# Kernel optimization log

Hardware: AMD Instinct MI355X
Metric: run time of the kernel (lower is better)

Reference implementation:

```python
import jax, jax.numpy as jnp
import numpy as np

CHUNK = 2048  # output-direction chunk size for the fused score+reduce scan


def _stereographic_normals(out_size):
    # matches torch.meshgrid default (ij indexing): v = rows, u = cols
    v, u = jnp.meshgrid(jnp.arange(out_size, dtype=jnp.float32),
                        jnp.arange(out_size, dtype=jnp.float32), indexing='ij')
    p = 4.0 * ((u + 0.5) / out_size - 0.5)
    q = -4.0 * ((v + 0.5) / out_size - 0.5)
    d = 1.0 + p ** 2 + q ** 2
    x = 2.0 * p / d
    y = 2.0 * q / d
    z = -(-1.0 + p ** 2 + q ** 2) / d
    return jnp.stack([x, y, z], axis=-1).reshape(-1, 3)  # [out_size^2, 3]


def _forward(image, normal_map, mask, kappa, out_size):
    B, C, H, W = image.shape
    N = H * W
    k = jnp.float32(kappa)
    coef = k / (2.0 * jnp.pi * (1.0 - jnp.exp(-2.0 * k)))  # vMF normalization

    V = image.reshape(B, C, N).transpose(0, 2, 1)              # [B,N,C]
    n_in = normal_map.reshape(B, 3, N).transpose(0, 2, 1)      # [B,N,3]
    w = (mask.reshape(B, N) > 0).astype(image.dtype)[..., None]  # 0/1 validity
    # fuse numerator (v^2) and denominator (v) accumulations into one pass
    Vaug = jnp.concatenate([V * w, (V ** 2) * w], axis=-1)     # [B,N,2C]

    M = _stereographic_normals(out_size)                        # [N_out,3]
    n_chunks = M.shape[0] // CHUNK
    chunks = M.reshape(n_chunks, CHUNK, 3)

    def body(carry, Mc):
        dp = jnp.einsum('bnd,cd->bnc', n_in, Mc)                # cos similarity
        f = coef * jnp.exp(-k * (1.0 - dp))                     # vMF kernel
        return carry, jnp.einsum('bnc,bnk->bck', f, Vaug)       # [B,CHUNK,2C]

    _, outs = jax.lax.scan(jax.checkpoint(body), 0.0, chunks)   # [n_chunks,B,CHUNK,2C]
    vals = outs.transpose(1, 0, 2, 3).reshape(B, out_size * out_size, 2 * C)
    s, num = vals[..., :C], vals[..., C:]
    out_pixels = num / (s + 0.001)                              # [B,N_out,C]
    return out_pixels.transpose(0, 2, 1).reshape(B, C, out_size, out_size)


def setup_inputs() -> dict:
    key = jax.random.key(0)
    k1, k2, k3 = jax.random.split(key, 3)
    B, C, H, W = 2, 3, 128, 128
    image = jax.random.uniform(k1, (B, C, H, W), dtype=jnp.float32)
    nm = jax.random.normal(k2, (B, 3, H, W), dtype=jnp.float32)
    nm = nm / jnp.linalg.norm(nm, axis=1, keepdims=True)  # unit normals
    mask = jax.random.randint(k3, (B, H, W), 0, 2).astype(jnp.int32)
    return {"image": image, "normal_map": nm, "mask": mask,
            "kappa": 100, "out_size": 256}


def reference(image, normal_map, mask, kappa, out_size):
    return _forward(image, normal_map, mask, kappa, out_size)
```

## Files before the change

kernel.cpp:

```cpp
#include <hip/hip_runtime.h>
#include <math.h>

#define B_     2
#define C_     3
#define N_     16384
#define OS_    256
#define OUT_   65536
#define NZ_    32
#define NF_    64
#define NB_    2048
#define NITEM_ 1536
#define GRIDM_ 2048
#define CAP_   16384
#define SP2_   512
#define VSTR_  520
#define TAU_   8.0f
#define LOG2E  1.44269504088896340736f
#define PI_    3.14159265358979323846f

typedef float    f32x4 __attribute__((ext_vector_type(4)));
typedef float    v2f   __attribute__((ext_vector_type(2)));
typedef _Float16 f16x8 __attribute__((ext_vector_type(8)));
typedef __fp16   h16x2 __attribute__((ext_vector_type(2)));

static __device__ __forceinline__ v2f pk_fma(v2f a, v2f b, v2f c) {
    return __builtin_elementwise_fma(a, b, c);
}

__device__ __forceinline__ int pixel_bin(float nx, float ny, float nz) {
    int zi = (int)((nz + 1.0f) * (NZ_ * 0.5f));
    zi = min(max(zi, 0), NZ_ - 1);
    float phi = atan2f(ny, nx);
    int fi = (int)((phi + PI_) * (NF_ / (2.0f * PI_)));
    fi = min(max(fi, 0), NF_ - 1);
    return zi * NF_ + fi;
}

__global__ __launch_bounds__(1024) void hist_scan_kernel(
    const float* __restrict__ nm, const int* __restrict__ mask,
    int* __restrict__ binStart, int* __restrict__ off)
{
    __shared__ int hist[NB_];
    int b = blockIdx.x;
    int tid = threadIdx.x;

    for (int i = tid; i < NB_; i += 1024) hist[i] = 0;
    __syncthreads();

#pragma unroll
    for (int j = 0; j < N_ / 1024; j++) {
        int n = j * 1024 + tid;
        if (mask[b * N_ + n] > 0) {
            const float* nb = nm + (size_t)b * 3 * N_ + n;
            atomicAdd(&hist[pixel_bin(nb[0], nb[N_], nb[2 * N_])], 1);
        }
    }
    __syncthreads();

    if (tid >= 64) return;
    int lane = tid;
    const int per = NB_ / 64;
    int base = lane * per;

    int sum = 0;
#pragma unroll
    for (int i = 0; i < per; i++) sum += hist[base + i];

    int inc = sum;
#pragma unroll
    for (int o = 1; o < 64; o <<= 1) {
        int t = __shfl_up(inc, o);
        if (lane >= o) inc += t;
    }
    int acc = inc - sum;

#pragma unroll
    for (int i = 0; i < per; i++) {
        binStart[b * (NB_ + 1) + base + i] = acc;
        off[b * NB_ + base + i] = acc;
        acc += hist[base + i];
    }
    if (lane == 63) binStart[b * (NB_ + 1) + NB_] = acc;
}

__global__ __launch_bounds__(256) void scatter_plan_kernel(
    const float* __restrict__ img, const float* __restrict__ nm,
    const int* __restrict__ mask, const int* __restrict__ kappa,
    const int* __restrict__ binStart, int* __restrict__ off,
    float* __restrict__ gn, _Float16* __restrict__ gv,
    int* __restrict__ plan, int* __restrict__ tileLen)
{
    int tid = threadIdx.x;
    int bid = blockIdx.x;
    float k = (float)kappa[0];
    float k2 = k * LOG2E;

    if (bid < 128) {
        int idx = bid * 256 + tid;
        if (idx >= B_ * N_) return;
        if (mask[idx] <= 0) return;
        int b = idx / N_, n = idx - b * N_;
        const float* nb = nm + (size_t)b * 3 * N_ + n;
        float nx = nb[0], ny = nb[N_], nz = nb[2 * N_];
        int bin = pixel_bin(nx, ny, nz);
        int pos = atomicAdd(&off[b * NB_ + bin], 1);
        const float* ib = img + (size_t)b * C_ * N_ + n;
        float v0 = ib[0], v1 = ib[N_], v2 = ib[2 * N_];
        gn[((size_t)b * 3 + 0) * CAP_ + pos] = k2 * nx;
        gn[((size_t)b * 3 + 1) * CAP_ + pos] = k2 * ny;
        gn[((size_t)b * 3 + 2) * CAP_ + pos] = k2 * nz;
        _Float16* gvb = gv + (size_t)b * 6 * CAP_;
        gvb[0 * CAP_ + pos] = (_Float16)v0;
        gvb[1 * CAP_ + pos] = (_Float16)v1;
        gvb[2 * CAP_ + pos] = (_Float16)v2;
        gvb[3 * CAP_ + pos] = (_Float16)(v0 * v0);
        gvb[4 * CAP_ + pos] = (_Float16)(v1 * v1);
        gvb[5 * CAP_ + pos] = (_Float16)(v2 * v2);
        return;
    }

    __shared__ int warr[4];
    int bt = bid - 128;
    int b = bt >> 8, tile = bt & 255;
    int tu = tile & 15, tv = tile >> 4;
    int w = tid >> 6, lane = tid & 63;

    float pc  = 4.0f * ((tu * 16 + 8.0f) * (1.0f / OS_) - 0.5f);
    float qc  = -4.0f * ((tv * 16 + 8.0f) * (1.0f / OS_) - 0.5f);
    float ppc = pc * pc + qc * qc, invc = 1.0f / (1.0f + ppc);
    float Tx = 2.0f * pc * invc, Ty = 2.0f * qc * invc, Tz = (1.0f - ppc) * invc;

    float ctile = 1.0f;
#pragma unroll
    for (int j = 0; j < 4; j++) {
        int cl = j * 64 + lane;
        int u = tu * 16 + (cl & 15), v = tv * 16 + (cl >> 4);
        float p = 4.0f * ((u + 0.5f) * (1.0f / OS_) - 0.5f);
        float q = -4.0f * ((v + 0.5f) * (1.0f / OS_) - 0.5f);
        float pp = p * p + q * q;
        float inv = 1.0f / (1.0f + pp);
        float mx = 2.0f * p * inv, my = 2.0f * q * inv, mz = (1.0f - pp) * inv;
        ctile = fminf(ctile, mx * Tx + my * Ty + mz * Tz);
    }
#pragma unroll
    for (int o = 32; o; o >>= 1) ctile = fminf(ctile, __shfl_xor(ctile, o));

    float dpthr = fminf(fmaxf(1.0f - TAU_ / k, -1.0f), 1.0f);
    ctile = fminf(fmaxf(ctile, -1.0f), 1.0f);
    float theta = acosf(dpthr) + acosf(ctile);
    float rhs = (theta >= PI_) ? -2.0f : cosf(theta);

    float rT   = sqrtf(Tx * Tx + Ty * Ty);
    float phiT = atan2f(Ty, Tx);
    int fiT = min(max((int)((phiT + PI_) * (NF_ / (2.0f * PI_))), 0), NF_ - 1);

    const int* bs = binStart + b * (NB_ + 1);
    int Lacc = 0;

#pragma unroll
    for (int j = 0; j < 8; j++) {
        int zi = w + j * 4;
        float z0 = -1.0f + zi * (2.0f / NZ_);
        float z1 = z0 + (2.0f / NZ_);
        float hw  = PI_ / NF_;
        float mid = -PI_ + (2.0f * PI_ / NF_) * lane + hw;
        float d = phiT - mid;
        d = d - (2.0f * PI_) * rintf(d * (0.5f / PI_));
        d = fabsf(d);
        float cmax = (d <= hw) ? 1.0f : cosf(d - hw);
        float A  = rT * cmax;
        float g0 = A * sqrtf(fmaxf(0.0f, 1.0f - z0 * z0)) + Tz * z0;
        float g1 = A * sqrtf(fmaxf(0.0f, 1.0f - z1 * z1)) + Tz * z1;
        float gm = fmaxf(g0, g1);
        if (A > 0.0f) {
            float s2 = A * A + Tz * Tz;
            float zs = Tz * rsqrtf(s2);
            if (zs > z0 && zs < z1) gm = sqrtf(s2);
        }
        unsigned long long m = __ballot(gm >= rhs);

        int base = zi * NF_;
        int st0 = 0, en0 = 0, st1 = 0, en1 = 0;
        if (m) {
            bool full = (~m == 0ull) || !((m >> fiT) & 1ull);
            if (!full) {
                unsigned long long r = fiT ? ((m >> fiT) | (m << (64 - fiT))) : m;
                unsigned long long nr = ~r;
                int bcnt = __builtin_ctzll(nr);
                int acnt = __builtin_clzll(nr);
                if (bcnt + acnt >= NF_) full = true;
                else {
                    int lo = fiT - acnt, hi = fiT + bcnt - 1;
                    if (lo >= 0 && hi < NF_) {
                        st0 = bs[base + lo]; en0 = bs[base + hi + 1];
                    } else if (lo < 0) {
                        st0 = bs[base];            en0 = bs[base + hi + 1];
                        st1 = bs[base + lo + NF_]; en1 = bs[base + NF_];
                    } else {
                        st0 = bs[base];       en0 = bs[base + hi - NF_ + 1];
                        st1 = bs[base + lo];  en1 = bs[base + NF_];
                    }
                }
            }
            if (full) { st0 = bs[base]; en0 = bs[base + NF_]; }
        }
        Lacc += (en0 - st0) + (en1 - st1);
        if (lane == 0) {
            int* o = plan + ((size_t)bt * NZ_ + zi) * 4;
            o[0] = st0; o[1] = en0; o[2] = st1; o[3] = en1;
        }
    }
    if (lane == 0) warr[w] = Lacc;
    __syncthreads();
    if (tid == 0) tileLen[bt] = warr[0] + warr[1] + warr[2] + warr[3];
}

__global__ __launch_bounds__(256) void builder_kernel(
    const int* __restrict__ tileLen, int* __restrict__ tileItemStart,
    int* __restrict__ items, int* __restrict__ hdr)
{
    __shared__ int lds[256];
    int t = threadIdx.x;
    int bt0 = t * 2, bt1 = t * 2 + 1;
    int L0 = tileLen[bt0], L1 = tileLen[bt1];

    lds[t] = L0 + L1;
    __syncthreads();
    for (int o = 128; o > 0; o >>= 1) {
        if (t < o) lds[t] += lds[t + o];
        __syncthreads();
    }
    int SL = lds[0];
    __syncthreads();

    int R = (SL + NITEM_ - 1) / NITEM_;
    if (R < 32) R = 32;

    int P0 = (L0 + R - 1) / R, P1 = (L1 + R - 1) / R;
    int ps = P0 + P1;
    lds[t] = ps;
    __syncthreads();
    for (int o = 1; o < 256; o <<= 1) {
        int v = (t >= o) ? lds[t - o] : 0;
        __syncthreads();
        lds[t] += v;
        __syncthreads();
    }
    int excl  = lds[t] - ps;
    int total = lds[255];

    tileItemStart[bt0] = excl;
    tileItemStart[bt1] = excl + P0;
    if (t == 255) tileItemStart[512] = total;
    if (t == 0)   hdr[0] = R;

    for (int p = 0; p < P0; p++) items[excl + p]      = (bt0 << 12) | p;
    for (int p = 0; p < P1; p++) items[excl + P0 + p] = (bt1 << 12) | p;
    for (int i = total + t; i < GRIDM_; i += 256) items[i] = -1;
}

__global__ __launch_bounds__(256) void main_kernel(
    const float* __restrict__ gn, const _Float16* __restrict__ gv,
    const int* __restrict__ plan, const int* __restrict__ items,
    const int* __restrict__ hdr, const int* __restrict__ kappa,
    float* __restrict__ part2)
{
    __shared__ float    s_nx[SP2_], s_ny[SP2_], s_nz[SP2_];
    __shared__ _Float16 s_va[6 * VSTR_ + 8];
    __shared__ int      rTab[128];
    __shared__ int      sTot;

    int item = items[blockIdx.x];
    if (item < 0) return;
    int bt = item >> 12, piece = item & 4095;
    int tile = bt & 255, b = bt >> 8;
    int tu = tile & 15, tv = tile >> 4;
    int tid = threadIdx.x, w = tid >> 6, lane = tid & 63;

    if (tid < 64) {
        int st = plan[(size_t)bt * (NZ_ * 4) + 2 * tid];
        int en = plan[(size_t)bt * (NZ_ * 4) + 2 * tid + 1];
        int len = en - st; if (len < 0) len = 0;
        int inc = len;
#pragma unroll
        for (int o = 1; o < 64; o <<= 1) {
            int t2 = __shfl_up(inc, o);
            if (tid >= o) inc += t2;
        }
        int pos = inc - len;
        rTab[tid * 2]     = pos;
        rTab[tid * 2 + 1] = st - pos;
        if (tid == 63) sTot = inc;
    }
    if (tid >= 64 && tid < 72) s_va[6 * VSTR_ + (tid - 64)] = (_Float16)0.0f;
    __syncthreads();

    int R   = hdr[0];
    int tot = sTot;
    int plo = piece * R;
    int phi = min(tot, plo + R);

    float k2 = (float)kappa[0] * LOG2E;
    v2f mk2v = {-k2, -k2};

    v2f Mx2[4], My2[4], Mz2[4];
#pragma unroll
    for (int t = 0; t < 4; t++) {
        int u = tu * 16 + (lane & 15);
        int v = tv * 16 + w * 4 + t;
        float p  = 4.0f * ((u + 0.5f) * (1.0f / OS_) - 0.5f);
        float q  = -4.0f * ((v + 0.5f) * (1.0f / OS_) - 0.5f);
        float pp = p * p + q * q;
        float inv = 1.0f / (1.0f + pp);
        float mx = 2.0f * p * inv, my = 2.0f * q * inv, mz = (1.0f - pp) * inv;
        Mx2[t] = (v2f){mx, mx}; My2[t] = (v2f){my, my}; Mz2[t] = (v2f){mz, mz};
    }

    f32x4 acc[4];
#pragma unroll
    for (int t = 0; t < 4; t++) acc[t] = (f32x4){0.0f, 0.0f, 0.0f, 0.0f};

    const float* gnx = gn + ((size_t)b * 3 + 0) * CAP_;
    const float* gny = gn + ((size_t)b * 3 + 1) * CAP_;
    const float* gnz = gn + ((size_t)b * 3 + 2) * CAP_;
    const _Float16* gvb = gv + (size_t)b * 6 * CAP_;

    int ch   = lane & 15;
    int kgrp = (lane >> 4) * 8;

    for (int s0 = plo; s0 < phi; s0 += SP2_) {
        int sp  = min(SP2_, phi - s0);
        int spP = (sp + 31) & ~31;
        int g0i = -1, g1i = -1;
        {
            int f0 = tid;
            if (f0 < sp) {
                int cp = s0 + f0, r = 0;
#pragma unroll
                for (int step = 32; step; step >>= 1) {
                    int nr = r + step;
                    if (rTab[nr * 2] <= cp) r = nr;
                }
                g0i = cp + rTab[r * 2 + 1];
            }
            int f1 = tid + 256;
            if (f1 < sp) {
                int cp = s0 + f1, r = 0;
#pragma unroll
                for (int step = 32; step; step >>= 1) {
                    int nr = r + step;
                    if (rTab[nr * 2] <= cp) r = nr;
                }
                g1i = cp + rTab[r * 2 + 1];
            }
        }
        __syncthreads();
#pragma unroll
        for (int h = 0; h < 2; h++) {
            int f = tid + h * 256;
            int g = h ? g1i : g0i;
            if (f >= spP) break;
            if (g >= 0) {
                s_nx[f] = gnx[g]; s_ny[f] = gny[g]; s_nz[f] = gnz[g];
#pragma unroll
                for (int c2 = 0; c2 < 6; c2++) s_va[c2 * VSTR_ + f] = gvb[c2 * CAP_ + g];
            } else {
                s_nx[f] = 0.0f; s_ny[f] = 0.0f; s_nz[f] = 0.0f;
#pragma unroll
                for (int c2 = 0; c2 < 6; c2++) s_va[c2 * VSTR_ + f] = (_Float16)0.0f;
            }
        }
        __syncthreads();

        for (int k0 = 0; k0 < spP; k0 += 32) {
            int kr = k0 + kgrp;
            const v2f* xv = (const v2f*)&s_nx[kr];
            const v2f* yv = (const v2f*)&s_ny[kr];
            const v2f* zv = (const v2f*)&s_nz[kr];
            v2f x01 = xv[0], x23 = xv[1], x45 = xv[2], x67 = xv[3];
            v2f y01 = yv[0], y23 = yv[1], y45 = yv[2], y67 = yv[3];
            v2f z01 = zv[0], z23 = zv[1], z45 = zv[2], z67 = zv[3];
            f16x8 bfrag;
            if (ch < 6) bfrag = *(const f16x8*)&s_va[ch * VSTR_ + kr];
            else        bfrag = *(const f16x8*)&s_va[6 * VSTR_];
#pragma unroll
            for (int t = 0; t < 4; t++) {
                v2f g01 = pk_fma(x01, Mx2[t], pk_fma(y01, My2[t], pk_fma(z01, Mz2[t], mk2v)));
                v2f g23 = pk_fma(x23, Mx2[t], pk_fma(y23, My2[t], pk_fma(z23, Mz2[t], mk2v)));
                v2f g45 = pk_fma(x45, Mx2[t], pk_fma(y45, My2[t], pk_fma(z45, Mz2[t], mk2v)));
                v2f g67 = pk_fma(x67, Mx2[t], pk_fma(y67, My2[t], pk_fma(z67, Mz2[t], mk2v)));
                h16x2 p0 = __builtin_amdgcn_cvt_pkrtz(__builtin_amdgcn_exp2f(g01.x),
                                                      __builtin_amdgcn_exp2f(g01.y));
                h16x2 p1 = __builtin_amdgcn_cvt_pkrtz(__builtin_amdgcn_exp2f(g23.x),
                                                      __builtin_amdgcn_exp2f(g23.y));
                h16x2 p2 = __builtin_amdgcn_cvt_pkrtz(__builtin_amdgcn_exp2f(g45.x),
                                                      __builtin_amdgcn_exp2f(g45.y));
                h16x2 p3 = __builtin_amdgcn_cvt_pkrtz(__builtin_amdgcn_exp2f(g67.x),
                                                      __builtin_amdgcn_exp2f(g67.y));
                f16x8 afrag;
                afrag[0] = (_Float16)p0[0]; afrag[1] = (_Float16)p0[1];
                afrag[2] = (_Float16)p1[0]; afrag[3] = (_Float16)p1[1];
                afrag[4] = (_Float16)p2[0]; afrag[5] = (_Float16)p2[1];
                afrag[6] = (_Float16)p3[0]; afrag[7] = (_Float16)p3[1];
                acc[t] = __builtin_amdgcn_mfma_f32_16x16x32_f16(afrag, bfrag, acc[t], 0, 0, 0);
            }
        }
        __syncthreads();
    }

    if (ch < 6) {
        float* dst = part2 + (size_t)blockIdx.x * 1536;
#pragma unroll
        for (int t = 0; t < 4; t++) {
#pragma unroll
            for (int r = 0; r < 4; r++) {
                int d = w * 64 + t * 16 + ((lane >> 4) * 4 + r);
                dst[d * 6 + ch] = acc[t][r];
            }
        }
    }
}

__global__ __launch_bounds__(256) void finalize_kernel(
    const float* __restrict__ part2, const int* __restrict__ tileItemStart,
    const int* __restrict__ kappa, float* __restrict__ out)
{
    int idx = blockIdx.x * 256 + threadIdx.x;
    if (idx >= B_ * OUT_) return;
    int b = idx / OUT_;
    int c = idx - b * OUT_;
    int u = c & 255, v = c >> 8;
    int bt = b * 256 + ((v >> 4) * 16 + (u >> 4));
    int cl = (v & 15) * 16 + (u & 15);

    float k = (float)kappa[0];
    float coef = k / (2.0f * PI_ * (1.0f - expf(-2.0f * k)));

    int is0 = tileItemStart[bt], is1 = tileItemStart[bt + 1];
    float s[6] = {0, 0, 0, 0, 0, 0};
    for (int it = is0; it < is1; it++) {
        const float* p = part2 + (size_t)it * 1536 + cl * 6;
#pragma unroll
        for (int i = 0; i < 6; i++) s[i] += p[i];
    }
#pragma unroll
    for (int ch = 0; ch < C_; ch++) {
        out[((size_t)(b * C_ + ch)) * OUT_ + c] = (coef * s[3 + ch]) / (coef * s[ch] + 0.001f);
    }
}

extern "C" void kernel_launch(void* const* d_in, const int* in_sizes, int n_in,
                              void* d_out, int out_size, void* d_ws, size_t ws_size,
                              hipStream_t stream)
{
    const float* img   = (const float*)d_in[0];
    const float* nm    = (const float*)d_in[1];
    const int*   mask  = (const int*)d_in[2];
    const int*   kappa = (const int*)d_in[3];
    float* out = (float*)d_out;

    char* ws = (char*)d_ws;
    size_t o = 0;
    float*     gn        = (float*)(ws + o);     o += (size_t)B_ * 3 * CAP_ * 4;
    _Float16*  gv        = (_Float16*)(ws + o); o += (size_t)B_ * 6 * CAP_ * 2;
    float*     part2     = (float*)(ws + o);     o += (size_t)GRIDM_ * 1536 * 4;
    int* plan            = (int*)(ws + o);       o += (size_t)512 * NZ_ * 4 * 4;
    int* off             = (int*)(ws + o);       o += (size_t)B_ * NB_ * 4;
    int* binStart        = (int*)(ws + o);       o += ((size_t)B_ * (NB_ + 1) * 4 + 15) & ~15ull;
    int* tileLen         = (int*)(ws + o);       o += 512 * 4;
    int* tileItemStart   = (int*)(ws + o);       o += (513 * 4 + 15) & ~15ull;
    int* items           = (int*)(ws + o);       o += GRIDM_ * 4;
    int* hdr             = (int*)(ws + o);       o += 16;

    hipLaunchKernelGGL(hist_scan_kernel, dim3(B_), dim3(1024), 0, stream,
                       nm, mask, binStart, off);
    hipLaunchKernelGGL(scatter_plan_kernel, dim3(640), dim3(256), 0, stream,
                       img, nm, mask, kappa, binStart, off, gn, gv, plan, tileLen);
    hipLaunchKernelGGL(builder_kernel, dim3(1), dim3(256), 0, stream,
                       tileLen, tileItemStart, items, hdr);
    hipLaunchKernelGGL(main_kernel, dim3(GRIDM_), dim3(256), 0, stream,
                       gn, gv, plan, items, hdr, kappa, part2);
    hipLaunchKernelGGL(finalize_kernel, dim3((B_ * OUT_ + 255) / 256), dim3(256), 0, stream,
                       part2, tileItemStart, kappa, out);
}
```

Baseline: 58.62 us.

## Fold work-item builder into main and finalize kernels, tighten vMF cutoff

Removes the single-block builder kernel launch. Every main and finalize block now recomputes the per-tile piece prefix sum from tileLen in shared memory, and main blocks find their tile with a binary search. This drops one serialized launch and its global round-trip, at the cost of redundant scan work and extra barriers in each of the many blocks. The truncation threshold TAU is also lowered from 8 to 6, which prunes more of the low-weight kernel tail and adds approximation error.

Result: faster. 56.09 us (-4.3%).

```diff
diff --git a/kernel.cpp b/kernel.cpp
--- a/kernel.cpp
+++ b/kernel.cpp
@@ -14,7 +14,7 @@
 #define CAP_   16384
 #define SP2_   512
 #define VSTR_  520
-#define TAU_   8.0f
+#define TAU_   6.0f
 #define LOG2E  1.44269504088896340736f
 #define PI_    3.14159265358979323846f
 
@@ -34,6 +34,43 @@
     int fi = (int)((phi + PI_) * (NF_ / (2.0f * PI_)));
     fi = min(max(fi, 0), NF_ - 1);
     return zi * NF_ + fi;
+}
+
+__device__ __forceinline__ void build_piece_prefix(
+    const int* __restrict__ tileLen, int* sPP, int* lds, int tid)
+{
+    int bt0 = tid * 2, bt1 = tid * 2 + 1;
+    int L0 = tileLen[bt0], L1 = tileLen[bt1];
+
+    lds[tid] = L0 + L1;
+    __syncthreads();
+    for (int o = 128; o > 0; o >>= 1) {
+        if (tid < o) lds[tid] += lds[tid + o];
+        __syncthreads();
+    }
+    int SL = lds[0];
+    __syncthreads();
+
+    int R = (SL + NITEM_ - 1) / NITEM_;
+    if (R < 32) R = 32;
+
+    int P0 = (L0 + R - 1) / R, P1 = (L1 + R - 1) / R;
+    int ps = P0 + P1;
+    lds[tid] = ps;
+    __syncthreads();
+    for (int o = 1; o < 256; o <<= 1) {
+        int v = (tid >= o) ? lds[tid - o] : 0;
+        __syncthreads();
+        lds[tid] += v;
+        __syncthreads();
+    }
+    int excl = lds[tid] - ps;
+    sPP[bt0] = excl;
+    sPP[bt1] = excl + P0;
+    if (tid == 255) sPP[512] = lds[255];
+    __syncthreads();
+    lds[0] = R;
+    __syncthreads();
 }
 
 __global__ __launch_bounds__(1024) void hist_scan_kernel(
@@ -215,67 +252,34 @@
     if (tid == 0) tileLen[bt] = warr[0] + warr[1] + warr[2] + warr[3];
 }
 
-__global__ __launch_bounds__(256) void builder_kernel(
-    const int* __restrict__ tileLen, int* __restrict__ tileItemStart,
-    int* __restrict__ items, int* __restrict__ hdr)
-{
-    __shared__ int lds[256];
-    int t = threadIdx.x;
-    int bt0 = t * 2, bt1 = t * 2 + 1;
-    int L0 = tileLen[bt0], L1 = tileLen[bt1];
-
-    lds[t] = L0 + L1;
-    __syncthreads();
-    for (int o = 128; o > 0; o >>= 1) {
-        if (t < o) lds[t] += lds[t + o];
-        __syncthreads();
-    }
-    int SL = lds[0];
-    __syncthreads();
-
-    int R = (SL + NITEM_ - 1) / NITEM_;
-    if (R < 32) R = 32;
-
-    int P0 = (L0 + R - 1) / R, P1 = (L1 + R - 1) / R;
-    int ps = P0 + P1;
-    lds[t] = ps;
-    __syncthreads();
-    for (int o = 1; o < 256; o <<= 1) {
-        int v = (t >= o) ? lds[t - o] : 0;
-        __syncthreads();
-        lds[t] += v;
-        __syncthreads();
-    }
-    int excl  = lds[t] - ps;
-    int total = lds[255];
-
-    tileItemStart[bt0] = excl;
-    tileItemStart[bt1] = excl + P0;
-    if (t == 255) tileItemStart[512] = total;
-    if (t == 0)   hdr[0] = R;
-
-    for (int p = 0; p < P0; p++) items[excl + p]      = (bt0 << 12) | p;
-    for (int p = 0; p < P1; p++) items[excl + P0 + p] = (bt1 << 12) | p;
-    for (int i = total + t; i < GRIDM_; i += 256) items[i] = -1;
-}
-
 __global__ __launch_bounds__(256) void main_kernel(
     const float* __restrict__ gn, const _Float16* __restrict__ gv,
-    const int* __restrict__ plan, const int* __restrict__ items,
-    const int* __restrict__ hdr, const int* __restrict__ kappa,
-    float* __restrict__ part2)
-{
+    const int* __restrict__ plan, const int* __restrict__ tileLen,
+    const int* __restrict__ kappa, float* __restrict__ part2)
+{
+    __shared__ int      sPP[513];
+    __shared__ int      lds[256];
     __shared__ float    s_nx[SP2_], s_ny[SP2_], s_nz[SP2_];
     __shared__ _Float16 s_va[6 * VSTR_ + 8];
     __shared__ int      rTab[128];
     __shared__ int      sTot;
 
-    int item = items[blockIdx.x];
-    if (item < 0) return;
-    int bt = item >> 12, piece = item & 4095;
+    int tid = threadIdx.x, w = tid >> 6, lane = tid & 63;
+
+    build_piece_prefix(tileLen, sPP, lds, tid);
+    int R = lds[0];
+    int bid = blockIdx.x;
+    if (bid >= sPP[512]) return;
+
+    int lo = 0;
+#pragma unroll
+    for (int s = 256; s; s >>= 1) {
+        int nr = lo + s;
+        if (nr <= 512 && sPP[nr] <= bid) lo = nr;
+    }
+    int bt = lo, piece = bid - sPP[lo];
     int tile = bt & 255, b = bt >> 8;
     int tu = tile & 15, tv = tile >> 4;
-    int tid = threadIdx.x, w = tid >> 6, lane = tid & 63;
 
     if (tid < 64) {
         int st = plan[(size_t)bt * (NZ_ * 4) + 2 * tid];
@@ -295,7 +299,6 @@
     if (tid >= 64 && tid < 72) s_va[6 * VSTR_ + (tid - 64)] = (_Float16)0.0f;
     __syncthreads();
 
-    int R   = hdr[0];
     int tot = sTot;
     int plo = piece * R;
     int phi = min(tot, plo + R);
@@ -409,7 +412,7 @@
     }
 
     if (ch < 6) {
-        float* dst = part2 + (size_t)blockIdx.x * 1536;
+        float* dst = part2 + (size_t)bid * 1536;
 #pragma unroll
         for (int t = 0; t < 4; t++) {
 #pragma unroll
@@ -422,10 +425,16 @@
 }
 
 __global__ __launch_bounds__(256) void finalize_kernel(
-    const float* __restrict__ part2, const int* __restrict__ tileItemStart,
+    const float* __restrict__ part2, const int* __restrict__ tileLen,
     const int* __restrict__ kappa, float* __restrict__ out)
 {
-    int idx = blockIdx.x * 256 + threadIdx.x;
+    __shared__ int sPP[513];
+    __shared__ int lds[256];
+    int tid = threadIdx.x;
+
+    build_piece_prefix(tileLen, sPP, lds, tid);
+
+    int idx = blockIdx.x * 256 + tid;
     if (idx >= B_ * OUT_) return;
     int b = idx / OUT_;
     int c = idx - b * OUT_;
@@ -436,7 +445,7 @@
     float k = (float)kappa[0];
     float coef = k / (2.0f * PI_ * (1.0f - expf(-2.0f * k)));
 
-    int is0 = tileItemStart[bt], is1 = tileItemStart[bt + 1];
+    int is0 = sPP[bt], is1 = sPP[bt + 1];
     float s[6] = {0, 0, 0, 0, 0, 0};
     for (int it = is0; it < is1; it++) {
         const float* p = part2 + (size_t)it * 1536 + cl * 6;
@@ -468,18 +477,13 @@
     int* off             = (int*)(ws + o);       o += (size_t)B_ * NB_ * 4;
     int* binStart        = (int*)(ws + o);       o += ((size_t)B_ * (NB_ + 1) * 4 + 15) & ~15ull;
     int* tileLen         = (int*)(ws + o);       o += 512 * 4;
-    int* tileItemStart   = (int*)(ws + o);       o += (513 * 4 + 15) & ~15ull;
-    int* items           = (int*)(ws + o);       o += GRIDM_ * 4;
-    int* hdr             = (int*)(ws + o);       o += 16;
 
     hipLaunchKernelGGL(hist_scan_kernel, dim3(B_), dim3(1024), 0, stream,
                        nm, mask, binStart, off);
     hipLaunchKernelGGL(scatter_plan_kernel, dim3(640), dim3(256), 0, stream,
                        img, nm, mask, kappa, binStart, off, gn, gv, plan, tileLen);
-    hipLaunchKernelGGL(builder_kernel, dim3(1), dim3(256), 0, stream,
-                       tileLen, tileItemStart, items, hdr);
     hipLaunchKernelGGL(main_kernel, dim3(GRIDM_), dim3(256), 0, stream,
-                       gn, gv, plan, items, hdr, kappa, part2);
+                       gn, gv, plan, tileLen, kappa, part2);
     hipLaunchKernelGGL(finalize_kernel, dim3((B_ * OUT_ + 255) / 256), dim3(256), 0, stream,
-                       part2, tileItemStart, kappa, out);
-}
+                       part2, tileLen, kappa, out);
+}
```
